# Kernel optimization log

Hardware: AMD Instinct MI355X
Metric: run time of the kernel (lower is better)

Reference implementation:

```python
import jax, jax.numpy as jnp
import numpy as np

DEPTH, DIM, HEADS, DH, MLP, N, B = 6, 192, 12, 16, 768, 256, 32
INNER = HEADS * DH  # 192


def setup_inputs() -> dict:
    key = jax.random.key(0)
    ks = jax.random.split(key, 10)
    w = lambda i, shape: jax.random.normal(ks[i], shape, dtype=jnp.float32) * 0.02
    return {
        'x': jax.random.normal(ks[0], (B, N, DIM), dtype=jnp.float32),
        'ln1_g': jnp.ones((DEPTH, DIM), jnp.float32),
        'ln1_b': jnp.zeros((DEPTH, DIM), jnp.float32),
        'Wq': w(1, (DEPTH, DIM, INNER)),
        'Wkv': w(2, (DEPTH, DIM, 2 * INNER)),
        'lsa_scale': jnp.full((DEPTH, HEADS), DH ** -0.5, dtype=jnp.float32),
        'mix_pre': jax.random.normal(ks[3], (DEPTH, HEADS, HEADS), dtype=jnp.float32),
        'mix_post': jax.random.normal(ks[4], (DEPTH, HEADS, HEADS), dtype=jnp.float32),
        'Wo': w(5, (DEPTH, INNER, DIM)),
        'bo': jnp.zeros((DEPTH, DIM), jnp.float32),
        'ls1': jnp.full((DEPTH, DIM), 0.1, dtype=jnp.float32),
        'ln2_g': jnp.ones((DEPTH, DIM), jnp.float32),
        'ln2_b': jnp.zeros((DEPTH, DIM), jnp.float32),
        'W1': w(6, (DEPTH, DIM, MLP)),
        'b1': jnp.zeros((DEPTH, MLP), jnp.float32),
        'W2': w(7, (DEPTH, MLP, DIM)),
        'b2': jnp.zeros((DEPTH, DIM), jnp.float32),
        'ls2': jnp.full((DEPTH, DIM), 0.1, dtype=jnp.float32),
    }


def _ln(x, g, b, eps=1e-5):
    m = x.mean(-1, keepdims=True)
    v = ((x - m) ** 2).mean(-1, keepdims=True)
    return (x - m) * jax.lax.rsqrt(v + eps) * g + b


def _heads(t, b, n):
    # (b, n, h*d) -> (b, h, n, d)
    return t.reshape(b, n, HEADS, DH).transpose(0, 2, 1, 3)


def _forward(x, ln1_g, ln1_b, Wq, Wkv, lsa_scale, mix_pre, mix_post, Wo, bo,
             ls1, ln2_g, ln2_b, W1, b1, W2, b2, ls2):
    b, n, _ = x.shape
    diag = jnp.arange(n)
    for l in range(DEPTH):
        # --- PreNorm + talking-heads LSA attention + LayerScale(0.1) ---
        h = _ln(x, ln1_g[l], ln1_b[l])
        q = _heads(h @ Wq[l], b, n)
        k, v = jnp.split(h @ Wkv[l], 2, axis=-1)
        k, v = _heads(k, b, n), _heads(v, b, n)
        dots = jnp.einsum('bhid,bhjd->bhij', q, k) * lsa_scale[l][None, :, None, None]
        # LSA: source sets diagonal to -1e-09 (literal, near-zero) when if_patch_attn
        dots = dots.at[:, :, diag, diag].set(-1e-9)
        dots = jnp.einsum('bhij,hg->bgij', dots, mix_pre[l])
        a = jax.nn.softmax(dots, axis=-1)
        a = jnp.einsum('bhij,hg->bgij', a, mix_post[l])
        o = jnp.einsum('bhij,bhjd->bhid', a, v)
        o = o.transpose(0, 2, 1, 3).reshape(b, n, INNER) @ Wo[l] + bo[l]
        x = x + o * ls1[l]
        # --- PreNorm + GELU FFN + LayerScale(0.1) ---
        h2 = _ln(x, ln2_g[l], ln2_b[l])
        f = jax.nn.gelu(h2 @ W1[l] + b1[l], approximate=False) @ W2[l] + b2[l]
        x = x + f * ls2[l]
    return x


def reference(x, ln1_g, ln1_b, Wq, Wkv, lsa_scale, mix_pre, mix_post, Wo, bo,
              ls1, ln2_g, ln2_b, W1, b1, W2, b2, ls2):
    return _forward(x, ln1_g, ln1_b, Wq, Wkv, lsa_scale, mix_pre, mix_post, Wo,
                    bo, ls1, ln2_g, ln2_b, W1, b1, W2, b2, ls2)
```

## Files before the change

kernel.cpp:

```cpp
#include <hip/hip_runtime.h>
#include <hip/hip_bf16.h>

#define DEPTH   6
#define DIM     192
#define HEADS   12
#define DH      16
#define MLPD    768
#define SEQ     256
#define BATCH   32
#define ROWS    (BATCH*SEQ)

typedef __attribute__((ext_vector_type(8))) short short8;
typedef __attribute__((ext_vector_type(4))) float f32x4;
typedef __attribute__((ext_vector_type(4))) _Float16 half4;
typedef __attribute__((ext_vector_type(8))) _Float16 half8;
typedef __hip_bfloat16 bf16_t;
typedef _Float16 f16_t;

__device__ __forceinline__ bf16_t f2b(float v){ return __float2bfloat16(v); }
__device__ __forceinline__ ushort f2u(float v){
    union{ bf16_t b; ushort u; } w; w.b = __float2bfloat16(v); return w.u;
}
__device__ __forceinline__ f16_t u2h(ushort u){ union{ ushort u; f16_t h; } w; w.u = u; return w.h; }
__device__ __forceinline__ ushort h2u(f16_t h){ union{ ushort u; f16_t h; } w; w.h = h; return w.u; }

__device__ __forceinline__ void async16(ushort* lds, const ushort* gp){
    __builtin_amdgcn_global_load_lds(
        (const __attribute__((address_space(1))) uint*)gp,
        (__attribute__((address_space(3))) uint*)lds, 16, 0, 0);
}

__global__ void copy_kernel(const float* __restrict__ x, float* __restrict__ xr, int n){
    int i = blockIdx.x*256 + threadIdx.x;
    if (i < n) xr[i] = x[i];
}

__device__ __forceinline__ void wt_tile(const float* __restrict__ W,
        ushort* __restrict__ WT, int K, int N, int l, int tx, int ty,
        int tid, ushort* T){
    const float* src = W + ((size_t)l*K + tx*64)*N + ty*64;
    ushort* dst = WT + ((size_t)l*N + ty*64)*K + tx*64;
    int r = tid >> 2, c4 = (tid & 3)*16;
    #pragma unroll
    for (int u=0; u<4; u++){
        float4 v = *(const float4*)(src + (size_t)r*N + c4 + u*4);
        T[(c4+u*4+0)*72 + r] = f2u(v.x);
        T[(c4+u*4+1)*72 + r] = f2u(v.y);
        T[(c4+u*4+2)*72 + r] = f2u(v.z);
        T[(c4+u*4+3)*72 + r] = f2u(v.w);
    }
    __syncthreads();
    int n = tid >> 2, k8 = (tid & 3)*16;
    #pragma unroll
    for (int u=0; u<2; u++)
        *(uint4*)(dst + (size_t)n*K + k8 + u*8) = *(uint4*)&T[n*72 + k8 + u*8];
}

__global__ __launch_bounds__(256) void wt_all(
        const float* __restrict__ Wq, const float* __restrict__ Wkv,
        const float* __restrict__ Wo, const float* __restrict__ W1,
        const float* __restrict__ W2,
        ushort* __restrict__ WqT, ushort* __restrict__ WkvT,
        ushort* __restrict__ WoT, ushort* __restrict__ W1T,
        ushort* __restrict__ W2T){
    __shared__ ushort T[64*72];
    int id = blockIdx.x, l = blockIdx.y, tid = threadIdx.x;
    if (id < 9)       wt_tile(Wq,  WqT,  192, 192, l, id/3,       id%3,       tid, T);
    else if (id < 27) wt_tile(Wkv, WkvT, 192, 384, l, (id-9)/6,   (id-9)%6,   tid, T);
    else if (id < 36) wt_tile(Wo,  WoT,  192, 192, l, (id-27)/3,  (id-27)%3,  tid, T);
    else if (id < 72) wt_tile(W1,  W1T,  192, 768, l, (id-36)/12, (id-36)%12, tid, T);
    else              wt_tile(W2,  W2T,  768, 192, l, (id-72)/3,  (id-72)%3,  tid, T);
}

template<int MODE, int NT>
__global__ __launch_bounds__(256) void gemm_ln_kernel(
        const float* __restrict__ xres, const float* __restrict__ ln_g,
        const float* __restrict__ ln_b, const ushort* __restrict__ BT0,
        const ushort* __restrict__ BT1, const float* __restrict__ bias,
        f16_t* __restrict__ out0, f16_t* __restrict__ out1){
    __shared__ ushort As[64*200];
    __shared__ ushort Bs[2][6*2048];
    int tid = threadIdx.x, lane = tid & 63, w = tid >> 6;
    int bm = blockIdx.x*64;
    int tile0 = blockIdx.y*NT;
    auto issueB = [&](int t, int buf){
        int bn = (tile0 + t)*64;
        const ushort* bt; int bnl;
        if (MODE == 0 && bn >= DIM){ bt = BT1; bnl = bn - DIM; }
        else { bt = BT0; bnl = bn; }
        const ushort* bp = bt + (size_t)(bnl + (tid>>2))*DIM + (tid&3)*8;
        #pragma unroll
        for (int c=0; c<6; c++)
            async16(&Bs[buf][c*2048 + tid*8], bp + c*32);
    };
    issueB(0, 0);
    float g0 = ln_g[lane], g1 = ln_g[lane+64], g2 = ln_g[lane+128];
    float e0 = ln_b[lane], e1 = ln_b[lane+64], e2 = ln_b[lane+128];
    for (int it = 0; it < 16; it++){
        int r = (w<<4) + it;
        const float* xr = xres + (size_t)(bm + r)*DIM;
        float v0 = xr[lane], v1 = xr[lane+64], v2 = xr[lane+128];
        float s = v0+v1+v2;
        #pragma unroll
        for (int off=32; off; off>>=1) s += __shfl_xor(s, off, 64);
        float m = s*(1.0f/192.0f);
        float d0=v0-m, d1=v1-m, d2=v2-m;
        float q = d0*d0+d1*d1+d2*d2;
        #pragma unroll
        for (int off=32; off; off>>=1) q += __shfl_xor(q, off, 64);
        float inv = rsqrtf(q*(1.0f/192.0f) + 1e-5f);
        ushort* dst = &As[r*200];
        dst[lane]     = f2u(d0*inv*g0 + e0);
        dst[lane+64]  = f2u(d1*inv*g1 + e1);
        dst[lane+128] = f2u(d2*inv*g2 + e2);
    }
    __syncthreads();
    int wrow = w >> 1, wcol = w & 1;
    int quad = lane >> 4, mr = lane & 15;
    for (int t = 0; t < NT; t++){
        if (t+1 < NT) issueB(t+1, (t+1)&1);
        const ushort* B = Bs[t&1];
        f32x4 acc[2][2] = {};
        #pragma unroll
        for (int c = 0; c < 6; c++){
            short8 a0 = *(const short8*)&As[(wrow*32+mr)*200    + c*32 + quad*8];
            short8 a1 = *(const short8*)&As[(wrow*32+16+mr)*200 + c*32 + quad*8];
            short8 b0 = *(const short8*)&B[c*2048 + (wcol*32+mr)*32    + quad*8];
            short8 b1 = *(const short8*)&B[c*2048 + (wcol*32+16+mr)*32 + quad*8];
            acc[0][0] = __builtin_amdgcn_mfma_f32_16x16x32_bf16(a0, b0, acc[0][0], 0,0,0);
            acc[0][1] = __builtin_amdgcn_mfma_f32_16x16x32_bf16(a0, b1, acc[0][1], 0,0,0);
            acc[1][0] = __builtin_amdgcn_mfma_f32_16x16x32_bf16(a1, b0, acc[1][0], 0,0,0);
            acc[1][1] = __builtin_amdgcn_mfma_f32_16x16x32_bf16(a1, b1, acc[1][1], 0,0,0);
        }
        int bn = (tile0 + t)*64;
        #pragma unroll
        for (int rr=0; rr<2; rr++){
            #pragma unroll
            for (int cc=0; cc<2; cc++){
                int col = bn + wcol*32 + cc*16 + mr;
                if (MODE == 0){
                    f16_t* op; size_t st;
                    if (col < DIM){ op = out0 + col; st = DIM; }
                    else          { op = out1 + (col - DIM); st = 2*DIM; }
                    #pragma unroll
                    for (int tt=0; tt<4; tt++){
                        int row = bm + wrow*32 + rr*16 + quad*4 + tt;
                        op[(size_t)row*st] = (f16_t)acc[rr][cc][tt];
                    }
                } else {
                    float bv = bias[col];
                    #pragma unroll
                    for (int tt=0; tt<4; tt++){
                        int row = bm + wrow*32 + rr*16 + quad*4 + tt;
                        float z = acc[rr][cc][tt] + bv;
                        ((bf16_t*)out0)[(size_t)row*MLPD + col] =
                            f2b(0.5f*z*(1.0f + erff(z*0.70710678118654752f)));
                    }
                }
            }
        }
        __syncthreads();
    }
}

template<int ROUNDS>
__global__ __launch_bounds__(256) void gemm_a_kernel(
        const ushort* __restrict__ A, const ushort* __restrict__ BT,
        const float* __restrict__ bias, const float* __restrict__ ls,
        float* __restrict__ xres){
    const int K = ROUNDS*192;
    __shared__ ushort As[6*2048];
    __shared__ ushort Bs[6*2048];
    int tid = threadIdx.x, lane = tid & 63, w = tid >> 6;
    int wrow = w >> 1, wcol = w & 1;
    int bm = blockIdx.x*64, bn = blockIdx.y*64;
    int quad = lane >> 4, mr = lane & 15;
    const ushort* ap = A  + (size_t)(bm + (tid>>2))*K + (tid&3)*8;
    const ushort* bp = BT + (size_t)(bn + (tid>>2))*K + (tid&3)*8;
    f32x4 acc[2][2] = {};
    for (int r = 0; r < ROUNDS; r++){
        #pragma unroll
        for (int c=0; c<6; c++){
            async16(&As[c*2048 + tid*8], ap + r*192 + c*32);
            async16(&Bs[c*2048 + tid*8], bp + r*192 + c*32);
        }
        __syncthreads();
        #pragma unroll
        for (int c=0; c<6; c++){
            short8 a0 = *(const short8*)&As[c*2048 + (wrow*32+mr)*32    + quad*8];
            short8 a1 = *(const short8*)&As[c*2048 + (wrow*32+16+mr)*32 + quad*8];
            short8 b0 = *(const short8*)&Bs[c*2048 + (wcol*32+mr)*32    + quad*8];
            short8 b1 = *(const short8*)&Bs[c*2048 + (wcol*32+16+mr)*32 + quad*8];
            acc[0][0] = __builtin_amdgcn_mfma_f32_16x16x32_bf16(a0, b0, acc[0][0], 0,0,0);
            acc[0][1] = __builtin_amdgcn_mfma_f32_16x16x32_bf16(a0, b1, acc[0][1], 0,0,0);
            acc[1][0] = __builtin_amdgcn_mfma_f32_16x16x32_bf16(a1, b0, acc[1][0], 0,0,0);
            acc[1][1] = __builtin_amdgcn_mfma_f32_16x16x32_bf16(a1, b1, acc[1][1], 0,0,0);
        }
        if (r+1 < ROUNDS) __syncthreads();
    }
    #pragma unroll
    for (int rr=0; rr<2; rr++){
        #pragma unroll
        for (int cc=0; cc<2; cc++){
            int col = bn + wcol*32 + cc*16 + mr;
            float bv = bias[col], lv = ls[col];
            #pragma unroll
            for (int tt=0; tt<4; tt++){
                int row = bm + wrow*32 + rr*16 + quad*4 + tt;
                xres[(size_t)row*DIM + col] += (acc[rr][cc][tt] + bv)*lv;
            }
        }
    }
}

#define SLAB    4488
#define IST     280
#define KV_OFF  53856
#define ROWP    200
#define Q_OFF   66656
#define POST_OFF 70112
#define PRE_OFF 71776
#define LTOT    71920

__global__ __launch_bounds__(1024, 1) void attn_kernel(
        const f16_t* __restrict__ qb, const f16_t* __restrict__ kvb,
        const float* __restrict__ lsa, const float* __restrict__ pre,
        const float* __restrict__ post, const ushort* __restrict__ WoT,
        const float* __restrict__ bo, const float* __restrict__ ls1,
        float* __restrict__ xres){
    __shared__ ushort L[LTOT];
    int tid  = threadIdx.x;
    int lane = tid & 63, w = tid >> 6;
    int quad = lane >> 4, nr = lane & 15;
    int b  = blockIdx.x >> 4;
    int i0 = (blockIdx.x & 15) << 4;

    {
        uint* Z = (uint*)&L[KV_OFF];
        for (int k = tid; k < (LTOT - KV_OFF)/2; k += 1024) Z[k] = 0;
    }
    __syncthreads();

    if (tid < 384){
        int e = tid*8, i = e/DIM, d = e%DIM, hh = d >> 4;
        float sc = lsa[hh];
        union { uint4 v; f16_t h[8]; } iv, ov;
        iv.v = *(const uint4*)(qb + (size_t)(b*SEQ + i0 + i)*DIM + d);
        #pragma unroll
        for (int u=0; u<8; u++) ov.h[u] = (f16_t)((float)iv.h[u]*sc);
        *(uint4*)&L[Q_OFF + i*ROWP + d] = ov.v;
    } else if (tid < 512){
        for (int k = tid-384; k < 256; k += 128){
            int gg = k >> 4, hh = k & 15;
            if (gg < 12 && hh < 12)
                L[POST_OFF + k] = h2u((f16_t)post[hh*12+gg]);
        }
    } else if (tid < 640){
        for (int k = tid-512; k < 144; k += 128)
            L[PRE_OFF + k] = h2u((f16_t)pre[k]);
    }
    auto stage_kv = [&](int c, int coloff){
        for (int u = tid; u < 1536; u += 1024){
            int e = u*8;
            int j = e/DIM, d = e%DIM;
            uint4 v = *(const uint4*)(kvb + (size_t)(b*SEQ + c*64 + j)*(2*DIM) + coloff + d);
            *(uint4*)&L[KV_OFF + j*ROWP + d] = v;
        }
    };
    __syncthreads();

    half4 postTf = *(const half4*)&L[POST_OFF + nr*16 + quad*4];

    {
        int jg = w*16 + nr;
        const f16_t* krow = kvb + (size_t)(b*SEQ + jg)*(2*DIM);
        half8 qh[6], kh[6];
        #pragma unroll
        for (int c=0; c<6; c++){
            union{ short8 s; half8 h; } a, k2;
            a.s  = *(const short8*)&L[Q_OFF + nr*ROWP + c*32 + quad*8];
            k2.s = *(const short8*)(const void*)(krow + c*32 + quad*8);
            qh[c] = a.h; kh[c] = k2.h;
        }
        int dd = jg - (i0 + quad*4);
        int hb = (quad>>1)*12;
        #pragma unroll
        for (int g=0; g<12; g++){
            f32x4 a = {0,0,0,0};
            #pragma unroll
            for (int c=0; c<6; c++){
                f16_t s = u2h(L[PRE_OFF + hb + c*24 + g]);
                a = __builtin_amdgcn_mfma_f32_16x16x32_f16(qh[c]*s, kh[c], a, 0,0,0);
            }
            ushort* sp = &L[g*SLAB + jg];
            sp[(quad*4+0)*IST] = (dd==0) ? (ushort)0 : h2u((f16_t)a[0]);
            sp[(quad*4+1)*IST] = (dd==1) ? (ushort)0 : h2u((f16_t)a[1]);
            sp[(quad*4+2)*IST] = (dd==2) ? (ushort)0 : h2u((f16_t)a[2]);
            sp[(quad*4+3)*IST] = (dd==3) ? (ushort)0 : h2u((f16_t)a[3]);
        }
    }
    __syncthreads();

    for (int r = w; r < 192; r += 16){
        int g = r >> 4, i = r & 15;
        ushort* sp = &L[g*SLAB + i*IST];
        ushort4 uv = *(ushort4*)&sp[lane*4];
        float e0 = __expf((float)u2h(uv.x));
        float e1 = __expf((float)u2h(uv.y));
        float e2 = __expf((float)u2h(uv.z));
        float e3 = __expf((float)u2h(uv.w));
        float ssum = e0+e1+e2+e3;
        #pragma unroll
        for (int off=32; off; off>>=1) ssum += __shfl_xor(ssum, off, 64);
        float rin = 1.0f/ssum;
        uv.x = h2u((f16_t)(e0*rin)); uv.y = h2u((f16_t)(e1*rin));
        uv.z = h2u((f16_t)(e2*rin)); uv.w = h2u((f16_t)(e3*rin));
        *(ushort4*)&sp[lane*4] = uv;
    }
    __syncthreads();

    for (int s = 0; s < 16; s++){
        int cb = s*16 + w;
        int i = cb >> 4, jb = cb & 15;
        int colbase = i*IST + jb*16 + nr;
        half4 bv;
        #pragma unroll
        for (int t=0; t<4; t++) bv[t] = u2h(L[(quad*4+t)*SLAB + colbase]);
        f32x4 cc = __builtin_amdgcn_mfma_f32_16x16x16f16(postTf, bv, (f32x4){0,0,0,0}, 0,0,0);
        if (quad < 3){
            #pragma unroll
            for (int t=0; t<4; t++) L[(quad*4+t)*SLAB + colbase] = h2u((f16_t)cc[t]);
        }
    }
    __syncthreads();

    f32x4 oacc = {0,0,0,0};
    for (int c = 0; c < 4; c++){
        stage_kv(c, DIM);
        __syncthreads();
        if (w < 12){
            int g = w;
            #pragma unroll
            for (int ks = 0; ks < 4; ks++){
                int jl = ks*16 + quad*4;
                half4 av = *(const half4*)&L[g*SLAB + nr*IST + c*64 + jl];
                half4 bv;
                #pragma unroll
                for (int t=0; t<4; t++) bv[t] = u2h(L[KV_OFF + (jl+t)*ROWP + g*16 + nr]);
                oacc = __builtin_amdgcn_mfma_f32_16x16x16f16(av, bv, oacc, 0,0,0);
            }
        }
        __syncthreads();
    }

    if (w < 12){
        int g = w;
        #pragma unroll
        for (int t=0; t<4; t++){
            int i = quad*4 + t;
            L[Q_OFF + i*ROWP + g*16 + nr] = f2u(oacc[t]);
        }
    }
    __syncthreads();

    if (w < 12){
        f32x4 wacc = {0,0,0,0};
        int ct = w;
        const ushort* wg = WoT + (size_t)(ct*16 + nr)*192;
        #pragma unroll
        for (int c = 0; c < 3; c++){
            #pragma unroll
            for (int sub = 0; sub < 2; sub++){
                int k0 = c*64 + sub*32;
                short8 av = *(const short8*)&L[Q_OFF + nr*ROWP + k0 + quad*8];
                short8 bv = *(const short8*)(wg + k0 + quad*8);
                wacc = __builtin_amdgcn_mfma_f32_16x16x32_bf16(av, bv, wacc, 0,0,0);
            }
        }
        int col = ct*16 + nr;
        float bv2 = bo[col], lv = ls1[col];
        #pragma unroll
        for (int t=0; t<4; t++){
            int row = b*SEQ + i0 + quad*4 + t;
            xres[(size_t)row*DIM + col] += (wacc[t] + bv2)*lv;
        }
    }
}

extern "C" void kernel_launch(void* const* d_in, const int* in_sizes, int n_in,
                              void* d_out, int out_size, void* d_ws, size_t ws_size,
                              hipStream_t stream){
    const float* x    = (const float*)d_in[0];
    const float* ln1g = (const float*)d_in[1];
    const float* ln1b = (const float*)d_in[2];
    const float* Wq   = (const float*)d_in[3];
    const float* Wkv  = (const float*)d_in[4];
    const float* lsa  = (const float*)d_in[5];
    const float* pre  = (const float*)d_in[6];
    const float* post = (const float*)d_in[7];
    const float* Wo   = (const float*)d_in[8];
    const float* bo   = (const float*)d_in[9];
    const float* ls1  = (const float*)d_in[10];
    const float* ln2g = (const float*)d_in[11];
    const float* ln2b = (const float*)d_in[12];
    const float* W1   = (const float*)d_in[13];
    const float* b1   = (const float*)d_in[14];
    const float* W2   = (const float*)d_in[15];
    const float* b2   = (const float*)d_in[16];
    const float* ls2  = (const float*)d_in[17];
    float* xres = (float*)d_out;

    char* ws = (char*)d_ws;
    f16_t*  qb  = (f16_t*)ws;
    f16_t*  kvb = (f16_t*)(ws + (size_t)ROWS*DIM*2);
    bf16_t* fb  = (bf16_t*)ws;
    char* p = ws + (size_t)ROWS*MLPD*2;
    ushort* WqT  = (ushort*)p; p += (size_t)DEPTH*DIM*DIM*2;
    ushort* WkvT = (ushort*)p; p += (size_t)DEPTH*DIM*2*DIM*2;
    ushort* WoT  = (ushort*)p; p += (size_t)DEPTH*DIM*DIM*2;
    ushort* W1T  = (ushort*)p; p += (size_t)DEPTH*DIM*MLPD*2;
    ushort* W2T  = (ushort*)p; p += (size_t)DEPTH*MLPD*DIM*2;

    int ntot = ROWS*DIM;
    copy_kernel<<<ntot/256, 256, 0, stream>>>(x, xres, ntot);
    wt_all<<<dim3(108, 6), 256, 0, stream>>>(Wq, Wkv, Wo, W1, W2,
                                             WqT, WkvT, WoT, W1T, W2T);
    for (int l = 0; l < DEPTH; l++){
        gemm_ln_kernel<0,3><<<dim3(128,3), 256, 0, stream>>>(xres,
                ln1g + l*DIM, ln1b + l*DIM,
                WqT + (size_t)l*DIM*DIM, WkvT + (size_t)l*DIM*2*DIM,
                nullptr, qb, kvb);
        attn_kernel<<<BATCH*(SEQ/16), 1024, 0, stream>>>(qb, kvb, lsa + l*HEADS,
                pre + l*HEADS*HEADS, post + l*HEADS*HEADS,
                WoT + (size_t)l*DIM*DIM, bo + l*DIM, ls1 + l*DIM, xres);
        gemm_ln_kernel<1,4><<<dim3(128,3), 256, 0, stream>>>(xres,
                ln2g + l*DIM, ln2b + l*DIM,
                W1T + (size_t)l*DIM*MLPD, nullptr, b1 + l*MLPD, (f16_t*)fb, nullptr);
        gemm_a_kernel<4><<<dim3(128,3), 256, 0, stream>>>((const ushort*)fb,
                W2T + (size_t)l*MLPD*DIM, b2 + l*DIM, ls2 + l*DIM, xres);
    }
}
```

Before: 703.9 us.

## Split LayerNorm into separate kernel and widen GEMM grid to one tile per block

Moves the LayerNorm out of the fused LN+GEMM kernel into a standalone ln_kernel that writes bf16 normalized rows to a workspace buffer. The GEMM then loads A and B tiles asynchronously and computes a single 64x64 output tile per block, growing the grid from 384 to over a thousand blocks. The aim is to stop recomputing LayerNorm for each column tile group and to give the GEMM more parallelism and smaller shared memory per block. In exchange it adds two kernel launches per layer and an extra global write and read of the normalized activations.

```diff
diff --git a/kernel.cpp b/kernel.cpp
--- a/kernel.cpp
+++ b/kernel.cpp
@@ -72,94 +72,92 @@
     else              wt_tile(W2,  W2T,  768, 192, l, (id-72)/3,  (id-72)%3,  tid, T);
 }
 
-template<int MODE, int NT>
+__global__ __launch_bounds__(256) void ln_kernel(
+        const float* __restrict__ xres, const float* __restrict__ ln_g,
+        const float* __restrict__ ln_b, ushort* __restrict__ out){
+    int lane = threadIdx.x & 63, w = threadIdx.x >> 6;
+    int row = blockIdx.x*4 + w;
+    const float* xr = xres + (size_t)row*DIM;
+    float v0 = xr[lane], v1 = xr[lane+64], v2 = xr[lane+128];
+    float s = v0+v1+v2;
+    #pragma unroll
+    for (int off=32; off; off>>=1) s += __shfl_xor(s, off, 64);
+    float m = s*(1.0f/192.0f);
+    float d0=v0-m, d1=v1-m, d2=v2-m;
+    float q = d0*d0+d1*d1+d2*d2;
+    #pragma unroll
+    for (int off=32; off; off>>=1) q += __shfl_xor(q, off, 64);
+    float inv = rsqrtf(q*(1.0f/192.0f) + 1e-5f);
+    float g0 = ln_g[lane], g1 = ln_g[lane+64], g2 = ln_g[lane+128];
+    float e0 = ln_b[lane], e1 = ln_b[lane+64], e2 = ln_b[lane+128];
+    ushort* dst = out + (size_t)row*DIM;
+    dst[lane]     = f2u(d0*inv*g0 + e0);
+    dst[lane+64]  = f2u(d1*inv*g1 + e1);
+    dst[lane+128] = f2u(d2*inv*g2 + e2);
+}
+
+template<int MODE>
 __global__ __launch_bounds__(256) void gemm_ln_kernel(
-        const float* __restrict__ xres, const float* __restrict__ ln_g,
-        const float* __restrict__ ln_b, const ushort* __restrict__ BT0,
+        const ushort* __restrict__ Aln, const ushort* __restrict__ BT0,
         const ushort* __restrict__ BT1, const float* __restrict__ bias,
         f16_t* __restrict__ out0, f16_t* __restrict__ out1){
-    __shared__ ushort As[64*200];
-    __shared__ ushort Bs[2][6*2048];
+    __shared__ ushort As[6*2048];
+    __shared__ ushort Bs[6*2048];
     int tid = threadIdx.x, lane = tid & 63, w = tid >> 6;
     int bm = blockIdx.x*64;
-    int tile0 = blockIdx.y*NT;
-    auto issueB = [&](int t, int buf){
-        int bn = (tile0 + t)*64;
+    int bn = blockIdx.y*64;
+    {
+        const ushort* ap = Aln + (size_t)(bm + (tid>>2))*DIM + (tid&3)*8;
         const ushort* bt; int bnl;
         if (MODE == 0 && bn >= DIM){ bt = BT1; bnl = bn - DIM; }
         else { bt = BT0; bnl = bn; }
         const ushort* bp = bt + (size_t)(bnl + (tid>>2))*DIM + (tid&3)*8;
         #pragma unroll
-        for (int c=0; c<6; c++)
-            async16(&Bs[buf][c*2048 + tid*8], bp + c*32);
-    };
-    issueB(0, 0);
-    float g0 = ln_g[lane], g1 = ln_g[lane+64], g2 = ln_g[lane+128];
-    float e0 = ln_b[lane], e1 = ln_b[lane+64], e2 = ln_b[lane+128];
-    for (int it = 0; it < 16; it++){
-        int r = (w<<4) + it;
-        const float* xr = xres + (size_t)(bm + r)*DIM;
-        float v0 = xr[lane], v1 = xr[lane+64], v2 = xr[lane+128];
-        float s = v0+v1+v2;
-        #pragma unroll
-        for (int off=32; off; off>>=1) s += __shfl_xor(s, off, 64);
-        float m = s*(1.0f/192.0f);
-        float d0=v0-m, d1=v1-m, d2=v2-m;
-        float q = d0*d0+d1*d1+d2*d2;
-        #pragma unroll
-        for (int off=32; off; off>>=1) q += __shfl_xor(q, off, 64);
-        float inv = rsqrtf(q*(1.0f/192.0f) + 1e-5f);
-        ushort* dst = &As[r*200];
-        dst[lane]     = f2u(d0*inv*g0 + e0);
-        dst[lane+64]  = f2u(d1*inv*g1 + e1);
-        dst[lane+128] = f2u(d2*inv*g2 + e2);
+        for (int c=0; c<6; c++){
+            async16(&As[c*2048 + tid*8], ap + c*32);
+            async16(&Bs[c*2048 + tid*8], bp + c*32);
+        }
     }
     __syncthreads();
     int wrow = w >> 1, wcol = w & 1;
     int quad = lane >> 4, mr = lane & 15;
-    for (int t = 0; t < NT; t++){
-        if (t+1 < NT) issueB(t+1, (t+1)&1);
-        const ushort* B = Bs[t&1];
-        f32x4 acc[2][2] = {};
-        #pragma unroll
-        for (int c = 0; c < 6; c++){
-            short8 a0 = *(const short8*)&As[(wrow*32+mr)*200    + c*32 + quad*8];
-            short8 a1 = *(const short8*)&As[(wrow*32+16+mr)*200 + c*32 + quad*8];
-            short8 b0 = *(const short8*)&B[c*2048 + (wcol*32+mr)*32    + quad*8];
-            short8 b1 = *(const short8*)&B[c*2048 + (wcol*32+16+mr)*32 + quad*8];
-            acc[0][0] = __builtin_amdgcn_mfma_f32_16x16x32_bf16(a0, b0, acc[0][0], 0,0,0);
-            acc[0][1] = __builtin_amdgcn_mfma_f32_16x16x32_bf16(a0, b1, acc[0][1], 0,0,0);
-            acc[1][0] = __builtin_amdgcn_mfma_f32_16x16x32_bf16(a1, b0, acc[1][0], 0,0,0);
-            acc[1][1] = __builtin_amdgcn_mfma_f32_16x16x32_bf16(a1, b1, acc[1][1], 0,0,0);
-        }
-        int bn = (tile0 + t)*64;
-        #pragma unroll
-        for (int rr=0; rr<2; rr++){
-            #pragma unroll
-            for (int cc=0; cc<2; cc++){
-                int col = bn + wcol*32 + cc*16 + mr;
-                if (MODE == 0){
-                    f16_t* op; size_t st;
-                    if (col < DIM){ op = out0 + col; st = DIM; }
-                    else          { op = out1 + (col - DIM); st = 2*DIM; }
-                    #pragma unroll
-                    for (int tt=0; tt<4; tt++){
-                        int row = bm + wrow*32 + rr*16 + quad*4 + tt;
-                        op[(size_t)row*st] = (f16_t)acc[rr][cc][tt];
-                    }
-                } else {
-                    float bv = bias[col];
-                    #pragma unroll
-                    for (int tt=0; tt<4; tt++){
-                        int row = bm + wrow*32 + rr*16 + quad*4 + tt;
-                        float z = acc[rr][cc][tt] + bv;
-                        ((bf16_t*)out0)[(size_t)row*MLPD + col] =
-                            f2b(0.5f*z*(1.0f + erff(z*0.70710678118654752f)));
-                    }
+    f32x4 acc[2][2] = {};
+    #pragma unroll
+    for (int c = 0; c < 6; c++){
+        short8 a0 = *(const short8*)&As[c*2048 + (wrow*32+mr)*32    + quad*8];
+        short8 a1 = *(const short8*)&As[c*2048 + (wrow*32+16+mr)*32 + quad*8];
+        short8 b0 = *(const short8*)&Bs[c*2048 + (wcol*32+mr)*32    + quad*8];
+        short8 b1 = *(const short8*)&Bs[c*2048 + (wcol*32+16+mr)*32 + quad*8];
+        acc[0][0] = __builtin_amdgcn_mfma_f32_16x16x32_bf16(a0, b0, acc[0][0], 0,0,0);
+        acc[0][1] = __builtin_amdgcn_mfma_f32_16x16x32_bf16(a0, b1, acc[0][1], 0,0,0);
+        acc[1][0] = __builtin_amdgcn_mfma_f32_16x16x32_bf16(a1, b0, acc[1][0], 0,0,0);
+        acc[1][1] = __builtin_amdgcn_mfma_f32_16x16x32_bf16(a1, b1, acc[1][1], 0,0,0);
+    }
+    #pragma unroll
+    for (int rr=0; rr<2; rr++){
+        #pragma unroll
+        for (int cc=0; cc<2; cc++){
+            int col = bn + wcol*32 + cc*16 + mr;
+            if (MODE == 0){
+                f16_t* op; size_t st;
+                if (col < DIM){ op = out0 + col; st = DIM; }
+                else          { op = out1 + (col - DIM); st = 2*DIM; }
+                #pragma unroll
+                for (int tt=0; tt<4; tt++){
+                    int row = bm + wrow*32 + rr*16 + quad*4 + tt;
+                    op[(size_t)row*st] = (f16_t)acc[rr][cc][tt];
+                }
+            } else {
+                float bv = bias[col];
+                #pragma unroll
+                for (int tt=0; tt<4; tt++){
+                    int row = bm + wrow*32 + rr*16 + quad*4 + tt;
+                    float z = acc[rr][cc][tt] + bv;
+                    ((bf16_t*)out0)[(size_t)row*MLPD + col] =
+                        f2b(0.5f*z*(1.0f + erff(z*0.70710678118654752f)));
                 }
             }
         }
-        __syncthreads();
     }
 }
 
@@ -420,21 +418,22 @@
     ushort* WoT  = (ushort*)p; p += (size_t)DEPTH*DIM*DIM*2;
     ushort* W1T  = (ushort*)p; p += (size_t)DEPTH*DIM*MLPD*2;
     ushort* W2T  = (ushort*)p; p += (size_t)DEPTH*MLPD*DIM*2;
+    ushort* lnb  = (ushort*)p; p += (size_t)ROWS*DIM*2;
 
     int ntot = ROWS*DIM;
     copy_kernel<<<ntot/256, 256, 0, stream>>>(x, xres, ntot);
     wt_all<<<dim3(108, 6), 256, 0, stream>>>(Wq, Wkv, Wo, W1, W2,
                                              WqT, WkvT, WoT, W1T, W2T);
     for (int l = 0; l < DEPTH; l++){
-        gemm_ln_kernel<0,3><<<dim3(128,3), 256, 0, stream>>>(xres,
-                ln1g + l*DIM, ln1b + l*DIM,
+        ln_kernel<<<ROWS/4, 256, 0, stream>>>(xres, ln1g + l*DIM, ln1b + l*DIM, lnb);
+        gemm_ln_kernel<0><<<dim3(128,9), 256, 0, stream>>>(lnb,
                 WqT + (size_t)l*DIM*DIM, WkvT + (size_t)l*DIM*2*DIM,
                 nullptr, qb, kvb);
         attn_kernel<<<BATCH*(SEQ/16), 1024, 0, stream>>>(qb, kvb, lsa + l*HEADS,
                 pre + l*HEADS*HEADS, post + l*HEADS*HEADS,
                 WoT + (size_t)l*DIM*DIM, bo + l*DIM, ls1 + l*DIM, xres);
-        gemm_ln_kernel<1,4><<<dim3(128,3), 256, 0, stream>>>(xres,
-                ln2g + l*DIM, ln2b + l*DIM,
+        ln_kernel<<<ROWS/4, 256, 0, stream>>>(xres, ln2g + l*DIM, ln2b + l*DIM, lnb);
+        gemm_ln_kernel<1><<<dim3(128,12), 256, 0, stream>>>(lnb,
                 W1T + (size_t)l*DIM*MLPD, nullptr, b1 + l*MLPD, (f16_t*)fb, nullptr);
         gemm_a_kernel<4><<<dim3(128,3), 256, 0, stream>>>((const ushort*)fb,
                 W2T + (size_t)l*MLPD*DIM, b2 + l*DIM, ls2 + l*DIM, xres);
```

After: 619.4 us. -12.0%, faster.
